# Optimization experiments

Hardware: AMD Instinct MI355X
Metric: run time of the kernel (lower is better)

The kernel has to match this reference:

```python
import jax, jax.numpy as jnp
import numpy as np
import math

E = 768      # embed_size
H = 12       # heads
D = E // H   # head_dim = 64
MAXLEN = 512
N = 8        # batch
L = 512      # seq_len (q_len == k_len)


def _sinusoid_table():
    # (2*MAXLEN-1, E) sinusoidal table, sin at even dims, cos at odd dims
    pos = jnp.arange(2 * MAXLEN - 1, dtype=jnp.float32)[:, None]
    div = jnp.exp(jnp.arange(0, E, 2, dtype=jnp.float32) * (-math.log(10000.0) / E))
    ang = pos * div  # (2M-1, E/2)
    return jnp.stack([jnp.sin(ang), jnp.cos(ang)], axis=-1).reshape(2 * MAXLEN - 1, E)


def setup_inputs() -> dict:
    key = jax.random.key(0)
    ks = jax.random.split(key, 16)
    sc = 0.02
    return {
        "values": jax.random.normal(ks[0], (N, L, E), jnp.float32),
        "keys": jax.random.normal(ks[1], (N, L, E), jnp.float32),
        "query": jax.random.normal(ks[2], (N, L, E), jnp.float32),
        "Wq": jax.random.normal(ks[3], (E, E), jnp.float32) * sc,
        "bq": jax.random.normal(ks[4], (E,), jnp.float32) * sc,
        "Wk": jax.random.normal(ks[5], (E, E), jnp.float32) * sc,
        "bk": jax.random.normal(ks[6], (E,), jnp.float32) * sc,
        "Wv": jax.random.normal(ks[7], (E, E), jnp.float32) * sc,
        "bv": jax.random.normal(ks[8], (E,), jnp.float32) * sc,
        "Wo": jax.random.normal(ks[9], (E, E), jnp.float32) * sc,
        "bo": jax.random.normal(ks[10], (E,), jnp.float32) * sc,
        "Wpos": jax.random.normal(ks[11], (E, E), jnp.float32) * sc,
        "bpos": jax.random.normal(ks[12], (E,), jnp.float32) * sc,
        "r_w_bias": jax.random.normal(ks[13], (H, D), jnp.float32),
        "r_r_bias": jax.random.normal(ks[14], (H, D), jnp.float32),
    }


def _rel_shift(x):
    # Faithful to the torch code: pad one row on q dim, shape-preserving view,
    # drop first row -> identity as written.
    xp = jnp.pad(x, ((0, 0), (0, 0), (1, 0), (0, 0)))
    return xp[:, :, 1:, :]


def reference(values, keys, query, Wq, bq, Wk, bk, Wv, bv, Wo, bo, Wpos, bpos, r_w_bias, r_r_bias):
    pe = _sinusoid_table()  # (2M-1, E)
    r = jnp.arange(L)
    idx = jnp.clip(r[:, None] - r[None, :] + (MAXLEN - 1), 0, 2 * MAXLEN - 2)  # (L, L)
    rel = pe[idx] @ Wpos + bpos                       # (L, L, E)
    rel = rel.reshape(L, L, H, D).transpose(2, 0, 1, 3)  # (H, L, L, D)

    q = (query @ Wq + bq).reshape(N, L, H, D)
    k = (keys @ Wk + bk).reshape(N, L, H, D)
    v = (values @ Wv + bv).reshape(N, L, H, D)

    ac = jnp.einsum('nqhd,nkhd->nhqk', q + r_w_bias[None, None], k)
    bd = jnp.einsum('nqhd,hqkd->nhqk', q + r_r_bias[None, None], rel)
    bd = _rel_shift(bd)

    scores = (ac + bd) / math.sqrt(D)
    attn = jax.nn.softmax(scores, axis=-1)
    out = jnp.einsum('nhqk,nkhd->nqhd', attn, v).reshape(N, L, E)
    return out @ Wo + bo
```

## Files before the change

### kernel.cpp

```cpp
#include <hip/hip_runtime.h>

typedef unsigned short u16;
typedef unsigned int u32;
typedef __bf16 bf16x8 __attribute__((ext_vector_type(8)));
typedef float f32x4 __attribute__((ext_vector_type(4)));

#define EMB 768
#define NH 12
#define HD 64
#define SEQ 512
#define NB 8
#define NLROWS 4096
#define PEROWS 1024

__device__ __forceinline__ float b2f(u16 u) {
    return __uint_as_float(((u32)u) << 16);
}
__device__ __forceinline__ u16 f2b(float f) {
    u32 x = __float_as_uint(f);
    u32 r = x + 0x7fffu + ((x >> 16) & 1u);
    return (u16)(r >> 16);
}
__device__ __forceinline__ u32 pack2(float a, float b) {
    return (u32)f2b(a) | ((u32)f2b(b) << 16);
}
__device__ __forceinline__ void gl_lds16(const u16* g, u16* l) {
    __builtin_amdgcn_global_load_lds((const __attribute__((address_space(1))) u32*)g,
                                     (__attribute__((address_space(3))) u32*)l, 16, 0, 0);
}

__global__ __launch_bounds__(256) void prep(
        const float* __restrict__ Wq, const float* __restrict__ Wk, const float* __restrict__ Wv,
        const float* __restrict__ Wo, const float* __restrict__ Wpos,
        u16* __restrict__ Wt, u16* __restrict__ pe,
        const float* __restrict__ q, const float* __restrict__ k, const float* __restrict__ v,
        u16* __restrict__ qc, u16* __restrict__ kc, u16* __restrict__ vc) {
    __shared__ u16 tile[32][33];
    int b = blockIdx.x;
    int tid = threadIdx.x;
    if (b < 2880) {
        int m = b / 576, r = b % 576;
        const float* src = (m == 0) ? Wq : (m == 1) ? Wk : (m == 2) ? Wv : (m == 3) ? Wo : Wpos;
        u16* dst = Wt + (size_t)m * EMB * EMB;
        int bx = (r % 24) * 32, by = (r / 24) * 32;
        int tx = tid & 31, ty = tid >> 5;
#pragma unroll
        for (int i = 0; i < 32; i += 8)
            tile[ty + i][tx] = f2b(src[(size_t)(by + ty + i) * EMB + bx + tx]);
        __syncthreads();
#pragma unroll
        for (int i = 0; i < 32; i += 8)
            dst[(size_t)(bx + ty + i) * EMB + by + tx] = tile[tx][ty + i];
    } else if (b < 3904) {
        int pos = b - 2880;
        int p2 = pos > 1022 ? 1022 : pos;
#pragma unroll
        for (int j = 0; j < 3; j++) {
            int col = tid + j * 256;
            int i = col >> 1;
            float ang = (float)p2 * expf(-0.023985261384f * (float)i);
            float val = (col & 1) ? cosf(ang) : sinf(ang);
            pe[(size_t)pos * EMB + col] = f2b(val);
        }
    } else {
        int idx = b - 3904;
        int w = idx / 1536, bx = idx % 1536;
        const float* s = (w == 0) ? q : (w == 1) ? k : v;
        u16* d = (w == 0) ? qc : (w == 1) ? kc : vc;
        size_t i = ((size_t)bx * 256 + tid) * 8;
        float4 f0 = *(const float4*)(s + i);
        float4 f1 = *(const float4*)(s + i + 4);
        uint4 o;
        o.x = pack2(f0.x, f0.y); o.y = pack2(f0.z, f0.w);
        o.z = pack2(f1.x, f1.y); o.w = pack2(f1.z, f1.w);
        *(uint4*)(d + i) = o;
    }
}

template <int BM, int BN, int NZ, bool OUTF32>
__global__ __launch_bounds__(256, 3) void gemm_k(
        const u16* A0, const u16* A1, const u16* A2, const u16* A3,
        const u16* W0, const u16* W1, const u16* W2, const u16* W3,
        const float* f0, const float* f1, const float* f2, const float* f3,
        void* C0, void* C1, void* C2, void* C3) {
    constexpr int RT = BM / 32;
    constexpr int CT = BN / 32;
    __shared__ __align__(16) u16 As[BM * 64];
    __shared__ __align__(16) u16 Bs[BN * 64];
    int z = (NZ > 1) ? blockIdx.z : 0;
    if (NZ > 1 && z == 3 && blockIdx.x >= PEROWS / BM) return;
    const u16* A = (z == 0) ? A0 : (z == 1) ? A1 : (z == 2) ? A2 : A3;
    const u16* Bt = (z == 0) ? W0 : (z == 1) ? W1 : (z == 2) ? W2 : W3;
    const float* bias = (z == 0) ? f0 : (z == 1) ? f1 : (z == 2) ? f2 : f3;
    void* Cv = (z == 0) ? C0 : (z == 1) ? C1 : (z == 2) ? C2 : C3;
    bool vtout = (NZ > 1) && (z == 2);

    int tid = threadIdx.x;
    int wave = tid >> 6, lane = tid & 63;
    int lrow = lane & 15, lq = lane >> 4;
    int lr8 = lane >> 3, lb = lane & 7;
    int m0 = blockIdx.x * BM, n0 = blockIdx.y * BN;
    int wr = (wave >> 1) * (BM / 2), wc = (wave & 1) * (BN / 2);
    const u16* Abase = A + (size_t)m0 * EMB + (size_t)(lb ^ lr8) * 8;
    const u16* Bbase = Bt + (size_t)n0 * EMB + (size_t)(lb ^ lr8) * 8;
    f32x4 acc[RT][CT] = {};

    for (int k0 = 0; k0 < EMB; k0 += 64) {
        __syncthreads();
#pragma unroll
        for (int j = 0; j < BM / 32; j++) {
            int row = j * 32 + wave * 8 + lr8;
            gl_lds16(Abase + (size_t)row * EMB + k0, &As[(j * 32 + wave * 8) * 64]);
        }
#pragma unroll
        for (int j = 0; j < BN / 32; j++) {
            int row = j * 32 + wave * 8 + lr8;
            gl_lds16(Bbase + (size_t)row * EMB + k0, &Bs[(j * 32 + wave * 8) * 64]);
        }
        __syncthreads();
#pragma unroll
        for (int ks = 0; ks < 2; ks++) {
            int pb = (ks * 4 + lq) ^ (lrow & 7);
            bf16x8 bfr[CT];
#pragma unroll
            for (int ct = 0; ct < CT; ct++)
                bfr[ct] = *(const bf16x8*)&Bs[(wc + ct * 16 + lrow) * 64 + pb * 8];
#pragma unroll
            for (int rt = 0; rt < RT; rt++) {
                bf16x8 afr = *(const bf16x8*)&As[(wr + rt * 16 + lrow) * 64 + pb * 8];
#pragma unroll
                for (int ct = 0; ct < CT; ct++)
                    acc[rt][ct] = __builtin_amdgcn_mfma_f32_16x16x32_bf16(afr, bfr[ct], acc[rt][ct], 0, 0, 0);
            }
        }
    }
#pragma unroll
    for (int rt = 0; rt < RT; rt++) {
#pragma unroll
        for (int ct = 0; ct < CT; ct++) {
            int col = n0 + wc + ct * 16 + lrow;
            float bvv = bias[col];
            int mrow = m0 + wr + rt * 16 + lq * 4;
            if (vtout) {
                int nb = mrow >> 9, kvl = mrow & 511;
                int hh = col >> 6, dl = col & 63;
                ushort4 pk;
                pk.x = f2b(acc[rt][ct][0] + bvv);
                pk.y = f2b(acc[rt][ct][1] + bvv);
                pk.z = f2b(acc[rt][ct][2] + bvv);
                pk.w = f2b(acc[rt][ct][3] + bvv);
                *(ushort4*)((u16*)Cv + (((size_t)(nb * NH + hh) * HD + dl) << 9) + kvl) = pk;
            } else if (OUTF32) {
#pragma unroll
                for (int r = 0; r < 4; r++)
                    ((float*)Cv)[(size_t)(mrow + r) * EMB + col] = acc[rt][ct][r] + bvv;
            } else {
#pragma unroll
                for (int r = 0; r < 4; r++)
                    ((u16*)Cv)[(size_t)(mrow + r) * EMB + col] = f2b(acc[rt][ct][r] + bvv);
            }
        }
    }
}

__global__ __launch_bounds__(256, 3) void attn_rpe(
        const u16* __restrict__ Qb, const u16* __restrict__ Kb, const u16* __restrict__ Vtg,
        const u16* __restrict__ Rb, const float* __restrict__ rwb, const float* __restrict__ rrb,
        u16* __restrict__ Ctx) {
    __shared__ __align__(16) u16 Ks[64 * 64];
    __shared__ __align__(16) u16 Vt[64 * 64];
    __shared__ __align__(16) u16 Rs[128 * 64];
    __shared__ __align__(16) u16 Psw[64 * 84];
    __shared__ __align__(16) u16 Pb[64 * 72];

    int q0 = blockIdx.x * 64;
    int h = blockIdx.y;
    int n = blockIdx.z;
    int tid = threadIdx.x;
    int wave = tid >> 6, lane = tid & 63;
    int lrow = lane & 15, lq = lane >> 4;
    int lr8 = lane >> 3, lb = lane & 7;
    int swz = (lb ^ lr8) * 8;

    bf16x8 aw[2], ar[2];
    {
        const u16* qrow = Qb + ((size_t)(n * SEQ + q0 + wave * 16 + lrow)) * EMB + h * HD;
#pragma unroll
        for (int ks = 0; ks < 2; ks++) {
            int c = ks * 32 + lq * 8;
            uint4 qv = *(const uint4*)(qrow + c);
            float4 w0 = *(const float4*)(rwb + h * HD + c);
            float4 w1 = *(const float4*)(rwb + h * HD + c + 4);
            float4 r0 = *(const float4*)(rrb + h * HD + c);
            float4 r1 = *(const float4*)(rrb + h * HD + c + 4);
            union { uint4 u; u16 s[8]; } qu; qu.u = qv;
            union { uint4 u; bf16x8 v; } ww, rr;
            ww.u.x = pack2(b2f(qu.s[0]) + w0.x, b2f(qu.s[1]) + w0.y);
            ww.u.y = pack2(b2f(qu.s[2]) + w0.z, b2f(qu.s[3]) + w0.w);
            ww.u.z = pack2(b2f(qu.s[4]) + w1.x, b2f(qu.s[5]) + w1.y);
            ww.u.w = pack2(b2f(qu.s[6]) + w1.z, b2f(qu.s[7]) + w1.w);
            rr.u.x = pack2(b2f(qu.s[0]) + r0.x, b2f(qu.s[1]) + r0.y);
            rr.u.y = pack2(b2f(qu.s[2]) + r0.z, b2f(qu.s[3]) + r0.w);
            rr.u.z = pack2(b2f(qu.s[4]) + r1.x, b2f(qu.s[5]) + r1.y);
            rr.u.w = pack2(b2f(qu.s[6]) + r1.z, b2f(qu.s[7]) + r1.w);
            aw[ks] = ww.v;
            ar[ks] = rr.v;
        }
    }

    auto stage_chunk = [&](int cc) {
#pragma unroll
        for (int j = 0; j < 2; j++) {
            int row = j * 32 + wave * 8 + lr8;
            gl_lds16(Kb + ((size_t)(n * SEQ + cc + row)) * EMB + h * HD + swz,
                     &Ks[(j * 32 + wave * 8) * 64]);
        }
#pragma unroll
        for (int j = 0; j < 2; j++) {
            int row = j * 32 + wave * 8 + lr8;
            gl_lds16(Vtg + (((size_t)(n * NH + h) * HD + row) << 9) + cc + swz,
                     &Vt[(j * 32 + wave * 8) * 64]);
        }
#pragma unroll
        for (int j = 0; j < 4; j++) {
            int row = j * 32 + wave * 8 + lr8;
            gl_lds16(Rb + (size_t)(q0 - cc + 448 + row) * EMB + h * HD + swz,
                     &Rs[(j * 32 + wave * 8) * 64]);
        }
    };

    float ls[4] = {0.f, 0.f, 0.f, 0.f};
    f32x4 acco[4] = {};

    stage_chunk(0);
    for (int c0 = 0; c0 < SEQ; c0 += 64) {
        __syncthreads();

        f32x4 sacc[4] = {};
        f32x4 pacc[5] = {};
        bf16x8 vf[2][4];
#pragma unroll
        for (int ks = 0; ks < 2; ks++) {
            int pb = (ks * 4 + lq) ^ (lrow & 7);
#pragma unroll
            for (int ct = 0; ct < 4; ct++) {
                bf16x8 bk = *(const bf16x8*)&Ks[(ct * 16 + lrow) * 64 + pb * 8];
                sacc[ct] = __builtin_amdgcn_mfma_f32_16x16x32_bf16(aw[ks], bk, sacc[ct], 0, 0, 0);
            }
#pragma unroll
            for (int jj = 0; jj < 5; jj++) {
                bf16x8 br = *(const bf16x8*)&Rs[((wave + jj) * 16 + lrow) * 64 + pb * 8];
                pacc[jj] = __builtin_amdgcn_mfma_f32_16x16x32_bf16(ar[ks], br, pacc[jj], 0, 0, 0);
            }
#pragma unroll
            for (int dt = 0; dt < 4; dt++)
                vf[ks][dt] = *(const bf16x8*)&Vt[(dt * 16 + lrow) * 64 + pb * 8];
        }
        __syncthreads();
        if (c0 + 64 < SEQ) stage_chunk(c0 + 64);

#pragma unroll
        for (int jj = 0; jj < 5; jj++)
#pragma unroll
            for (int r = 0; r < 4; r++)
                Psw[(wave * 16 + lq * 4 + r) * 84 + jj * 16 + lrow] = f2b(pacc[jj][r]);

#pragma unroll
        for (int ct = 0; ct < 4; ct++)
#pragma unroll
            for (int r = 0; r < 4; r++) {
                int qloc = wave * 16 + lq * 4 + r;
                int col = lq * 4 + r - (ct * 16 + lrow) + 63;
                float bd = b2f(Psw[qloc * 84 + col]);
                float p = exp2f((sacc[ct][r] + bd) * 0.18033688011f);
                ls[r] += p;
                Pb[qloc * 72 + ct * 16 + lrow] = f2b(p);
            }

#pragma unroll
        for (int ks = 0; ks < 2; ks++) {
            bf16x8 ap = *(const bf16x8*)&Pb[(wave * 16 + lrow) * 72 + ks * 32 + lq * 8];
#pragma unroll
            for (int dt = 0; dt < 4; dt++)
                acco[dt] = __builtin_amdgcn_mfma_f32_16x16x32_bf16(ap, vf[ks][dt], acco[dt], 0, 0, 0);
        }
    }

#pragma unroll
    for (int r = 0; r < 4; r++) {
#pragma unroll
        for (int msk = 1; msk < 16; msk <<= 1)
            ls[r] += __shfl_xor(ls[r], msk);
    }
#pragma unroll
    for (int r = 0; r < 4; r++) {
        float inv = 1.0f / ls[r];
#pragma unroll
        for (int dt = 0; dt < 4; dt++) {
            int q = q0 + wave * 16 + lq * 4 + r;
            int d = dt * 16 + lrow;
            Ctx[((size_t)(n * SEQ + q)) * EMB + h * HD + d] = f2b(acco[dt][r] * inv);
        }
    }
}

extern "C" void kernel_launch(void* const* d_in, const int* in_sizes, int n_in,
                              void* d_out, int out_size, void* d_ws, size_t ws_size,
                              hipStream_t stream) {
    const float* values = (const float*)d_in[0];
    const float* keys   = (const float*)d_in[1];
    const float* query  = (const float*)d_in[2];
    const float* Wq = (const float*)d_in[3];
    const float* bq = (const float*)d_in[4];
    const float* Wk = (const float*)d_in[5];
    const float* bk = (const float*)d_in[6];
    const float* Wv = (const float*)d_in[7];
    const float* bv = (const float*)d_in[8];
    const float* Wo = (const float*)d_in[9];
    const float* bo = (const float*)d_in[10];
    const float* Wpos = (const float*)d_in[11];
    const float* bpos = (const float*)d_in[12];
    const float* rwb = (const float*)d_in[13];
    const float* rrb = (const float*)d_in[14];
    float* out = (float*)d_out;

    u16* ws = (u16*)d_ws;
    size_t off = 0;
    u16* Wt = ws;            off += (size_t)5 * EMB * EMB;
    u16* pe = ws + off;      off += (size_t)PEROWS * EMB;
    u16* Rb = ws + off;      off += (size_t)PEROWS * EMB;
    u16* qc = ws + off;      off += (size_t)NLROWS * EMB;
    u16* kc = ws + off;      off += (size_t)NLROWS * EMB;
    u16* vc = ws + off;      off += (size_t)NLROWS * EMB;
    u16* Qp = ws + off;      off += (size_t)NLROWS * EMB;
    u16* Kp = ws + off;      off += (size_t)NLROWS * EMB;
    u16* Vtg = ws + off;     off += (size_t)NLROWS * EMB;
    u16* Cx = qc;

    prep<<<dim3(8512), dim3(256), 0, stream>>>(Wq, Wk, Wv, Wo, Wpos, Wt, pe,
                                               query, keys, values, qc, kc, vc);

    gemm_k<128, 128, 4, false><<<dim3(32, 6, 4), dim3(256), 0, stream>>>(
        qc, kc, vc, pe,
        Wt, Wt + (size_t)1 * EMB * EMB, Wt + (size_t)2 * EMB * EMB, Wt + (size_t)4 * EMB * EMB,
        bq, bk, bv, bpos,
        Qp, Kp, Vtg, Rb);

    attn_rpe<<<dim3(8, NH, NB), dim3(256), 0, stream>>>(Qp, Kp, Vtg, Rb, rwb, rrb, Cx);

    gemm_k<64, 96, 1, true><<<dim3(64, 8), dim3(256), 0, stream>>>(
        Cx, Cx, Cx, Cx,
        Wt + (size_t)3 * EMB * EMB, Wt + (size_t)3 * EMB * EMB,
        Wt + (size_t)3 * EMB * EMB, Wt + (size_t)3 * EMB * EMB,
        bo, bo, bo, bo,
        out, out, out, out);
}
```

Measured before the change: 180.8 us.

## Use per-wave transposed score scratch, vectorized stores, fast trig, retuned projection tiles

```diff
diff --git a/kernel.cpp b/kernel.cpp
--- a/kernel.cpp
+++ b/kernel.cpp
@@ -58,8 +58,8 @@
         for (int j = 0; j < 3; j++) {
             int col = tid + j * 256;
             int i = col >> 1;
-            float ang = (float)p2 * expf(-0.023985261384f * (float)i);
-            float val = (col & 1) ? cosf(ang) : sinf(ang);
+            float ang = (float)p2 * __expf(-0.023985261384f * (float)i);
+            float val = (col & 1) ? __cosf(ang) : __sinf(ang);
             pe[(size_t)pos * EMB + col] = f2b(val);
         }
     } else {
@@ -78,7 +78,7 @@
 }
 
 template <int BM, int BN, int NZ, bool OUTF32>
-__global__ __launch_bounds__(256, 3) void gemm_k(
+__global__ __launch_bounds__(256, 4) void gemm_k(
         const u16* A0, const u16* A1, const u16* A2, const u16* A3,
         const u16* W0, const u16* W1, const u16* W2, const u16* W3,
         const float* f0, const float* f1, const float* f2, const float* f3,
@@ -170,8 +170,7 @@
     __shared__ __align__(16) u16 Ks[64 * 64];
     __shared__ __align__(16) u16 Vt[64 * 64];
     __shared__ __align__(16) u16 Rs[128 * 64];
-    __shared__ __align__(16) u16 Psw[64 * 84];
-    __shared__ __align__(16) u16 Pb[64 * 72];
+    __shared__ __align__(16) u16 PsPb[4 * 1664];
 
     int q0 = blockIdx.x * 64;
     int h = blockIdx.y;
@@ -181,6 +180,7 @@
     int lrow = lane & 15, lq = lane >> 4;
     int lr8 = lane >> 3, lb = lane & 7;
     int swz = (lb ^ lr8) * 8;
+    u16* psd = &PsPb[wave * 1664];
 
     bf16x8 aw[2], ar[2];
     {
@@ -260,29 +260,36 @@
         if (c0 + 64 < SEQ) stage_chunk(c0 + 64);
 
 #pragma unroll
-        for (int jj = 0; jj < 5; jj++)
-#pragma unroll
-            for (int r = 0; r < 4; r++)
-                Psw[(wave * 16 + lq * 4 + r) * 84 + jj * 16 + lrow] = f2b(pacc[jj][r]);
-
+        for (int jj = 0; jj < 5; jj++) {
+            ushort4 pk;
+            pk.x = f2b(pacc[jj][0]); pk.y = f2b(pacc[jj][1]);
+            pk.z = f2b(pacc[jj][2]); pk.w = f2b(pacc[jj][3]);
+            *(ushort4*)&psd[(jj * 16 + lrow) * 20 + lq * 4] = pk;
+        }
+
+        float bd[4][4];
 #pragma unroll
         for (int ct = 0; ct < 4; ct++)
 #pragma unroll
             for (int r = 0; r < 4; r++) {
-                int qloc = wave * 16 + lq * 4 + r;
-                int col = lq * 4 + r - (ct * 16 + lrow) + 63;
-                float bd = b2f(Psw[qloc * 84 + col]);
-                float p = exp2f((sacc[ct][r] + bd) * 0.18033688011f);
+                int jwin = lq * 4 + r - (ct * 16 + lrow) + 63;
+                bd[ct][r] = b2f(psd[jwin * 20 + lq * 4 + r]);
+            }
+#pragma unroll
+        for (int ct = 0; ct < 4; ct++)
+#pragma unroll
+            for (int r = 0; r < 4; r++) {
+                float p = exp2f((sacc[ct][r] + bd[ct][r]) * 0.18033688011f);
                 ls[r] += p;
-                Pb[qloc * 72 + ct * 16 + lrow] = f2b(p);
+                psd[(lq * 4 + r) * 72 + ct * 16 + lrow] = f2b(p);
             }
 
 #pragma unroll
         for (int ks = 0; ks < 2; ks++) {
-            bf16x8 ap = *(const bf16x8*)&Pb[(wave * 16 + lrow) * 72 + ks * 32 + lq * 8];
+            bf16x8 pf = *(const bf16x8*)&psd[lrow * 72 + ks * 32 + lq * 8];
 #pragma unroll
             for (int dt = 0; dt < 4; dt++)
-                acco[dt] = __builtin_amdgcn_mfma_f32_16x16x32_bf16(ap, vf[ks][dt], acco[dt], 0, 0, 0);
+                acco[dt] = __builtin_amdgcn_mfma_f32_16x16x32_bf16(vf[ks][dt], pf, acco[dt], 0, 0, 0);
         }
     }
 
@@ -292,15 +299,22 @@
         for (int msk = 1; msk < 16; msk <<= 1)
             ls[r] += __shfl_xor(ls[r], msk);
     }
-#pragma unroll
-    for (int r = 0; r < 4; r++) {
-        float inv = 1.0f / ls[r];
-#pragma unroll
-        for (int dt = 0; dt < 4; dt++) {
-            int q = q0 + wave * 16 + lq * 4 + r;
-            int d = dt * 16 + lrow;
-            Ctx[((size_t)(n * SEQ + q)) * EMB + h * HD + d] = f2b(acco[dt][r] * inv);
-        }
+    float* lsb = (float*)Rs;
+    if (lrow == 0) {
+#pragma unroll
+        for (int r = 0; r < 4; r++)
+            lsb[wave * 16 + lq * 4 + r] = ls[r];
+    }
+    float inv = 1.0f / lsb[wave * 16 + lrow];
+    int q = q0 + wave * 16 + lrow;
+#pragma unroll
+    for (int dt = 0; dt < 4; dt++) {
+        ushort4 pk;
+        pk.x = f2b(acco[dt][0] * inv);
+        pk.y = f2b(acco[dt][1] * inv);
+        pk.z = f2b(acco[dt][2] * inv);
+        pk.w = f2b(acco[dt][3] * inv);
+        *(ushort4*)&Ctx[((size_t)(n * SEQ + q)) * EMB + h * HD + dt * 16 + lq * 4] = pk;
     }
 }
 
@@ -340,7 +354,7 @@
     prep<<<dim3(8512), dim3(256), 0, stream>>>(Wq, Wk, Wv, Wo, Wpos, Wt, pe,
                                                query, keys, values, qc, kc, vc);
 
-    gemm_k<128, 128, 4, false><<<dim3(32, 6, 4), dim3(256), 0, stream>>>(
+    gemm_k<128, 96, 4, false><<<dim3(32, 8, 4), dim3(256), 0, stream>>>(
         qc, kc, vc, pe,
         Wt, Wt + (size_t)1 * EMB * EMB, Wt + (size_t)2 * EMB * EMB, Wt + (size_t)4 * EMB * EMB,
         bq, bk, bv, bpos,
```

New measurement: 179.3 us. About the same (-0.8%).
